# Kernel tuning notes

Hardware: AMD Instinct MI355X
Metric: run time of the kernel (lower is better)

Reference implementation:

```python
import jax, jax.numpy as jnp
import numpy as np

N_CLI, N_AGG, E, D, L = 100000, 1000, 1600000, 128, 3


def setup_inputs() -> dict:
    key = jax.random.key(0)
    ks = jax.random.split(key, 16)
    inp = {
        'x_clients': jax.random.normal(ks[0], (N_CLI, D), jnp.float32),
        'x_agg': jax.random.normal(ks[1], (N_AGG, D), jnp.float32),
        'c2a_src': jax.random.randint(ks[2], (E,), 0, N_CLI, jnp.int32),
        'c2a_dst': jax.random.randint(ks[3], (E,), 0, N_AGG, jnp.int32),
        'a2c_src': jax.random.randint(ks[4], (E,), 0, N_AGG, jnp.int32),
        'a2c_dst': jax.random.randint(ks[5], (E,), 0, N_CLI, jnp.int32),
    }
    s = 1.0 / np.sqrt(D)
    # stacked per-layer SAGE params for each edge type: W_l (on aggregated msg), W_r (on dst), b
    inp['Wl_c2a'] = jax.random.uniform(ks[6], (L, D, D), jnp.float32, -s, s)
    inp['Wr_c2a'] = jax.random.uniform(ks[7], (L, D, D), jnp.float32, -s, s)
    inp['b_c2a'] = jax.random.uniform(ks[8], (L, D), jnp.float32, -s, s)
    inp['Wl_a2c'] = jax.random.uniform(ks[9], (L, D, D), jnp.float32, -s, s)
    inp['Wr_a2c'] = jax.random.uniform(ks[10], (L, D, D), jnp.float32, -s, s)
    inp['b_a2c'] = jax.random.uniform(ks[11], (L, D), jnp.float32, -s, s)
    inp['W_lin'] = jax.random.uniform(ks[12], (D, 1), jnp.float32, -s, s)
    inp['b_lin'] = jax.random.uniform(ks[13], (1,), jnp.float32, -s, s)
    return inp


def _sage(x_src, x_dst, src, dst, Wl, Wr, b, n_dst):
    # mean aggregation of gathered source features onto dst nodes
    msg = x_src[src]                                        # [E, D]
    summed = jax.ops.segment_sum(msg, dst, num_segments=n_dst)
    cnt = jax.ops.segment_sum(jnp.ones((src.shape[0], 1), x_src.dtype), dst, num_segments=n_dst)
    mean = summed / jnp.maximum(cnt, 1.0)
    return mean @ Wl + x_dst @ Wr + b


def _leaky(x):
    return jnp.where(x >= 0, x, 0.1 * x)


def reference(x_clients, x_agg, c2a_src, c2a_dst, a2c_src, a2c_dst,
              Wl_c2a, Wr_c2a, b_c2a, Wl_a2c, Wr_a2c, b_a2c, W_lin, b_lin):
    xc, xa = x_clients, x_agg
    for l in range(L):
        new_a = _sage(xc, xa, c2a_src, c2a_dst, Wl_c2a[l], Wr_c2a[l], b_c2a[l], N_AGG)
        new_c = _sage(xa, xc, a2c_src, a2c_dst, Wl_a2c[l], Wr_a2c[l], b_a2c[l], N_CLI)
        xa, xc = _leaky(new_a), _leaky(new_c)
    return (xc @ W_lin + b_lin).squeeze(1)
```

## Files before the change

### kernel.cpp

```cpp
#include <hip/hip_runtime.h>

#define D      128
#define NCLI   100000
#define NAGG   1000
#define NLAYER 3
#define NBKT   782
#define NRNG   8
#define NBIN   (NAGG * NRNG)
#define RMAGIC 343598u
#define NHIST  512
#define NCVTX  (NCLI * D / 4 / 256)
#define NCVTW  ((NLAYER * D * D + 255) / 256)
#define NROWT  (NCLI / 32)

typedef short bf16x8 __attribute__((ext_vector_type(8)));
typedef float f32x16 __attribute__((ext_vector_type(16)));

static __device__ __forceinline__ float leaky(float x) { return x >= 0.f ? x : 0.1f * x; }

static __device__ __forceinline__ unsigned bf16_rn(float f) {
    unsigned u = __float_as_uint(f);
    return (u + 0x7fffu + ((u >> 16) & 1u)) >> 16;
}
static __device__ __forceinline__ float bf_val(unsigned h) { return __uint_as_float(h << 16); }
static __device__ __forceinline__ unsigned pack_bf2(float lo, float hi) {
    return bf16_rn(lo) | (bf16_rn(hi) << 16);
}
static __device__ __forceinline__ float bf_lo(unsigned v) { return __uint_as_float(v << 16); }
static __device__ __forceinline__ float bf_hi(unsigned v) { return __uint_as_float(v & 0xffff0000u); }

__global__ __launch_bounds__(256) void prep(const int* __restrict__ c2a_src,
                                            const int* __restrict__ c2a_dst,
                                            const int* __restrict__ a2c_dst, int E,
                                            int* __restrict__ cnt_ar, int* __restrict__ bcnt,
                                            const float4* __restrict__ X4,
                                            uint2* __restrict__ xhi, uint2* __restrict__ xlo,
                                            const float* __restrict__ W,
                                            unsigned short* __restrict__ Wt) {
    __shared__ int h[NBIN + NBKT];
    int bid = blockIdx.x;
    if (bid < NHIST) {
        for (int i = threadIdx.x; i < NBIN + NBKT; i += 256) h[i] = 0;
        __syncthreads();
        int stride = NHIST * 256;
        for (int e = bid * 256 + threadIdx.x; e < E; e += stride) {
            int s = c2a_src[e];
            int bin = c2a_dst[e] * NRNG + (int)__umulhi((unsigned)s, RMAGIC);
            atomicAdd(&h[bin], 1);
            atomicAdd(&h[NBIN + (a2c_dst[e] >> 7)], 1);
        }
        __syncthreads();
        for (int i = threadIdx.x; i < NBIN; i += 256)
            if (h[i]) atomicAdd(&cnt_ar[i], h[i]);
        for (int i = threadIdx.x; i < NBKT; i += 256)
            if (h[NBIN + i]) atomicAdd(&bcnt[i], h[NBIN + i]);
    } else if (bid < NHIST + NCVTX) {
        int t = (bid - NHIST) * 256 + threadIdx.x;
        float4 f = X4[t];
        unsigned h0 = bf16_rn(f.x), h1 = bf16_rn(f.y), h2 = bf16_rn(f.z), h3 = bf16_rn(f.w);
        xhi[t] = make_uint2(h0 | (h1 << 16), h2 | (h3 << 16));
        xlo[t] = make_uint2(pack_bf2(f.x - bf_val(h0), f.y - bf_val(h1)),
                            pack_bf2(f.z - bf_val(h2), f.w - bf_val(h3)));
    } else {
        int idx = (bid - NHIST - NCVTX) * 256 + threadIdx.x;
        if (idx >= NLAYER * D * D) return;
        int layer = idx >> 14, rem = idx & (D * D - 1);
        int k = rem >> 7, n = rem & 127;
        float w = W[layer * D * D + k * D + n];
        unsigned hh = bf16_rn(w);
        unsigned short* base = Wt + layer * 2 * D * D;
        base[n * D + k] = (unsigned short)hh;
        base[D * D + n * D + k] = (unsigned short)bf16_rn(w - bf_val(hh));
    }
}

__global__ void scan_both(const int* __restrict__ cnt_ar, int* __restrict__ rp_ar,
                          int* __restrict__ cur_ar, const int* __restrict__ bcnt,
                          int* __restrict__ brp, int* __restrict__ bcur) {
    __shared__ int sh[1024];
    int t = threadIdx.x;
    if (blockIdx.x == 0) {
        int v[8];
        int s = 0;
#pragma unroll
        for (int j = 0; j < 8; j++) {
            int idx = t * 8 + j;
            v[j] = (idx < NBIN) ? cnt_ar[idx] : 0;
            s += v[j];
        }
        sh[t] = s;
        __syncthreads();
        for (int off = 1; off < 1024; off <<= 1) {
            int x = (t >= off) ? sh[t - off] : 0;
            __syncthreads();
            sh[t] += x;
            __syncthreads();
        }
        int run = sh[t] - s;
#pragma unroll
        for (int j = 0; j < 8; j++) {
            int idx = t * 8 + j;
            if (idx < NBIN) {
                rp_ar[idx] = run;
                cur_ar[idx] = run;
            }
            run += v[j];
        }
        if (t == 1023) rp_ar[NBIN] = sh[1023];
    } else {
        int v = (t < NBKT) ? bcnt[t] : 0;
        sh[t] = v;
        __syncthreads();
        for (int off = 1; off < 1024; off <<= 1) {
            int x = (t >= off) ? sh[t - off] : 0;
            __syncthreads();
            sh[t] += x;
            __syncthreads();
        }
        if (t == 0) { brp[0] = 0; bcur[0] = 0; }
        if (t < NBKT) {
            brp[t + 1] = sh[t];
            if (t + 1 < NBKT) bcur[t + 1] = sh[t];
        }
    }
}

__global__ __launch_bounds__(1024) void scatter_both(const int* __restrict__ c2a_src,
                                                     const int* __restrict__ c2a_dst,
                                                     const int* __restrict__ a2c_src,
                                                     const int* __restrict__ a2c_dst, int E,
                                                     int* __restrict__ cur_ar,
                                                     int* __restrict__ col_c2a,
                                                     int* __restrict__ bcur,
                                                     int* __restrict__ sorted1) {
    __shared__ int sbuf[2 * NBIN];
    int tid = threadIdx.x;
    if (blockIdx.x < 256) {
        int* h = sbuf;
        int* base = sbuf + NBIN;
        int chunk = (E + 255) / 256;
        int e0 = blockIdx.x * chunk;
        int e1 = min(E, e0 + chunk);
        for (int i = tid; i < NBIN; i += 1024) h[i] = 0;
        __syncthreads();
        for (int e = e0 + tid; e < e1; e += 1024) {
            int s = c2a_src[e];
            atomicAdd(&h[c2a_dst[e] * NRNG + (int)__umulhi((unsigned)s, RMAGIC)], 1);
        }
        __syncthreads();
        for (int i = tid; i < NBIN; i += 1024) {
            int c = h[i];
            base[i] = c ? atomicAdd(&cur_ar[i], c) : 0;
        }
        __syncthreads();
        for (int e = e0 + tid; e < e1; e += 1024) {
            int s = c2a_src[e];
            int bin = c2a_dst[e] * NRNG + (int)__umulhi((unsigned)s, RMAGIC);
            int pos = atomicAdd(&base[bin], 1);
            col_c2a[pos] = s;
        }
    } else {
        int* h = sbuf;
        int* base = sbuf + NBKT;
        int bid = blockIdx.x - 256;
        int chunk = (E + 255) / 256;
        int e0 = bid * chunk;
        int e1 = min(E, e0 + chunk);
        for (int i = tid; i < NBKT; i += 1024) h[i] = 0;
        __syncthreads();
        for (int e = e0 + tid; e < e1; e += 1024) atomicAdd(&h[a2c_dst[e] >> 7], 1);
        __syncthreads();
        for (int i = tid; i < NBKT; i += 1024) {
            int c = h[i];
            base[i] = c ? atomicAdd(&bcur[i], c) : 0;
        }
        __syncthreads();
        for (int e = e0 + tid; e < e1; e += 1024) {
            int d = a2c_dst[e];
            int pos = atomicAdd(&base[d >> 7], 1);
            sorted1[pos] = ((d & 127) << 10) | a2c_src[e];
        }
    }
}

__global__ __launch_bounds__(512) void bucket_csr(const int* __restrict__ brp,
                                                  const int* __restrict__ sorted1,
                                                  int* __restrict__ rp_c,
                                                  int* __restrict__ col) {
    __shared__ int h[128], cur[128];
    int b = blockIdx.x, tid = threadIdx.x;
    if (tid < 128) h[tid] = 0;
    __syncthreads();
    int beg = brp[b], end = brp[b + 1];
    for (int e = beg + tid; e < end; e += 512) atomicAdd(&h[sorted1[e] >> 10], 1);
    __syncthreads();
    if (tid < 128) cur[tid] = h[tid];
    __syncthreads();
    for (int off = 1; off < 128; off <<= 1) {
        int x = 0;
        if (tid < 128 && tid >= off) x = cur[tid - off];
        __syncthreads();
        if (tid < 128) cur[tid] += x;
        __syncthreads();
    }
    if (tid < 128) {
        int start = beg + cur[tid] - h[tid];
        int c = b * 128 + tid;
        if (c < NCLI) rp_c[c] = start;
        cur[tid] = start;
    }
    if (b == NBKT - 1 && tid == 0) rp_c[NCLI] = end;
    __syncthreads();
    for (int e = beg + tid; e < end; e += 512) {
        int p = sorted1[e];
        int pos = atomicAdd(&cur[p >> 10], 1);
        col[pos] = p & 1023;
    }
}


__global__ __launch_bounds__(512) void gather_mean(const unsigned* __restrict__ tbl,
                                                   const int* __restrict__ rp_ar,
                                                   const int* __restrict__ col,
                                                   float* __restrict__ psum) {
    __shared__ float part[4][8][D];
    int quad = blockIdx.x >> 3, r = blockIdx.x & 7;
    int tid = threadIdx.x;
    int a = tid >> 7;
    int sub = (tid >> 4) & 7;
    int sl = tid & 15;
    const uint4* tbl4 = (const uint4*)tbl;
    int agg = quad * 4 + a;
    int bin = agg * NRNG + r;
    int beg = rp_ar[bin], end = rp_ar[bin + 1];
    float f0 = 0, f1 = 0, f2 = 0, f3 = 0, f4 = 0, f5 = 0, f6 = 0, f7 = 0;
    int e = beg + sub;
    for (; e + 8 < end; e += 16) {
        int s0 = col[e];
        int s1 = col[e + 8];
        uint4 v0 = tbl4[(s0 << 4) + sl];
        uint4 v1 = tbl4[(s1 << 4) + sl];
        f0 += bf_lo(v0.x); f1 += bf_hi(v0.x); f2 += bf_lo(v0.y); f3 += bf_hi(v0.y);
        f4 += bf_lo(v0.z); f5 += bf_hi(v0.z); f6 += bf_lo(v0.w); f7 += bf_hi(v0.w);
        f0 += bf_lo(v1.x); f1 += bf_hi(v1.x); f2 += bf_lo(v1.y); f3 += bf_hi(v1.y);
        f4 += bf_lo(v1.z); f5 += bf_hi(v1.z); f6 += bf_lo(v1.w); f7 += bf_hi(v1.w);
    }
    if (e < end) {
        int s0 = col[e];
        uint4 v0 = tbl4[(s0 << 4) + sl];
        f0 += bf_lo(v0.x); f1 += bf_hi(v0.x); f2 += bf_lo(v0.y); f3 += bf_hi(v0.y);
        f4 += bf_lo(v0.z); f5 += bf_hi(v0.z); f6 += bf_lo(v0.w); f7 += bf_hi(v0.w);
    }
    float* pr = &part[a][sub][sl * 8];
    pr[0] = f0; pr[1] = f1; pr[2] = f2; pr[3] = f3;
    pr[4] = f4; pr[5] = f5; pr[6] = f6; pr[7] = f7;
    __syncthreads();
    int c = tid & 127;
    float s = 0.f;
#pragma unroll
    for (int g = 0; g < 8; g++) s += part[a][g][c];
    psum[((size_t)agg * NRNG + r) * D + c] = s;
}

__global__ __launch_bounds__(128) void combine_agg(const float* __restrict__ psum,
                                                   const int* __restrict__ rp_ar,
                                                   const float* xa_old,
                                                   const float* __restrict__ Wl_a2c,
                                                   const float* __restrict__ Wl_c2a,
                                                   const float* __restrict__ Wr_c2a,
                                                   const float* __restrict__ b_c2a,
                                                   unsigned short* __restrict__ ya_bf,
                                                   float* xa_out) {
    __shared__ float mr[D], xr[D];
    int i = blockIdx.x, j = threadIdx.x;
    const float* pr = psum + (size_t)i * NRNG * D + j;
    float s = 0.f;
#pragma unroll
    for (int r = 0; r < NRNG; r++) s += pr[r * D];
    int deg = rp_ar[i * NRNG + NRNG] - rp_ar[i * NRNG];
    mr[j] = s / fmaxf((float)deg, 1.f);
    xr[j] = xa_old[i * D + j];
    __syncthreads();
    float accy = 0.f, accn = b_c2a[j];
#pragma unroll 4
    for (int k = 0; k < D; k++) {
        accy += xr[k] * Wl_a2c[k * D + j];
        accn += mr[k] * Wl_c2a[k * D + j] + xr[k] * Wr_c2a[k * D + j];
    }
    ya_bf[i * D + j] = (unsigned short)bf16_rn(accy);
    xa_out[i * D + j] = leaky(accn);
}

__global__ __launch_bounds__(256) void gemm_mfma(const unsigned short* __restrict__ Ahi,
                                                 const unsigned short* __restrict__ Alo,
                                                 const unsigned short* __restrict__ Wt,
                                                 const float* __restrict__ bias,
                                                 float* __restrict__ Y) {
    int tid = threadIdx.x;
    int wave = tid >> 6, lane = tid & 63;
    int cl = lane & 31, kh = lane >> 5;
    int n0 = wave * 32;
    const unsigned short* Wlo = Wt + D * D;
    const unsigned short* wbh = Wt + (size_t)(n0 + cl) * D + kh * 8;
    const unsigned short* wbl = Wlo + (size_t)(n0 + cl) * D + kh * 8;
    bf16x8 bhi[8], blo[8];
#pragma unroll
    for (int kc = 0; kc < 8; kc++) {
        bhi[kc] = *(const bf16x8*)(wbh + kc * 16);
        blo[kc] = *(const bf16x8*)(wbl + kc * 16);
    }
    float bv = bias[n0 + cl];
    for (int r = blockIdx.x; r < NROWT; r += gridDim.x) {
        int m0 = r * 32;
        const unsigned short* ar = Ahi + (size_t)(m0 + cl) * D + kh * 8;
        const unsigned short* al = Alo + (size_t)(m0 + cl) * D + kh * 8;
        bf16x8 ahi[8], alo[8];
#pragma unroll
        for (int kc = 0; kc < 8; kc++) {
            ahi[kc] = *(const bf16x8*)(ar + kc * 16);
            alo[kc] = *(const bf16x8*)(al + kc * 16);
        }
        f32x16 acc;
#pragma unroll
        for (int q = 0; q < 16; q++) acc[q] = bv;
#pragma unroll
        for (int kc = 0; kc < 8; kc++) {
            acc = __builtin_amdgcn_mfma_f32_32x32x16_bf16(ahi[kc], bhi[kc], acc, 0, 0, 0);
            acc = __builtin_amdgcn_mfma_f32_32x32x16_bf16(alo[kc], bhi[kc], acc, 0, 0, 0);
            acc = __builtin_amdgcn_mfma_f32_32x32x16_bf16(ahi[kc], blo[kc], acc, 0, 0, 0);
        }
        float* yb = Y + (size_t)m0 * D + n0 + cl;
#pragma unroll
        for (int reg = 0; reg < 16; reg++) {
            int row = (reg & 3) + 8 * (reg >> 2) + 4 * kh;
            yb[(size_t)row * D] = acc[reg];
        }
    }
}

template <int LAST>
__global__ __launch_bounds__(256) void agg_c_bf(const unsigned* __restrict__ ya,
                                                const int* __restrict__ rowptr,
                                                const int* __restrict__ col,
                                                const float* __restrict__ Y,
                                                unsigned* __restrict__ xhi,
                                                unsigned* __restrict__ xlo,
                                                const float* __restrict__ Wlin,
                                                const float* __restrict__ blin,
                                                float* __restrict__ out, int E) {
    int l = threadIdx.x & 63;
    int gid = blockIdx.x * 4 + (threadIdx.x >> 6);
    if (gid >= NCLI) return;
    int beg = rowptr[gid], end = rowptr[gid + 1];
    float a0 = 0, b0 = 0, a1 = 0, b1 = 0, a2 = 0, b2 = 0, a3 = 0, b3 = 0;
    float a4 = 0, b4 = 0, a5 = 0, b5 = 0, a6 = 0, b6 = 0, a7 = 0, b7 = 0;
    for (int ch = beg; ch < end; ch += 64) {
        int len = min(64, end - ch);
        int ec = col[min(ch + l, E - 1)];
        int j = 0;
        for (; j + 8 <= len; j += 8) {
            int r0 = __shfl(ec, j + 0), r1 = __shfl(ec, j + 1);
            int r2 = __shfl(ec, j + 2), r3 = __shfl(ec, j + 3);
            int r4 = __shfl(ec, j + 4), r5 = __shfl(ec, j + 5);
            int r6 = __shfl(ec, j + 6), r7 = __shfl(ec, j + 7);
            unsigned v0 = ya[(r0 << 6) + l];
            unsigned v1 = ya[(r1 << 6) + l];
            unsigned v2 = ya[(r2 << 6) + l];
            unsigned v3 = ya[(r3 << 6) + l];
            unsigned v4 = ya[(r4 << 6) + l];
            unsigned v5 = ya[(r5 << 6) + l];
            unsigned v6 = ya[(r6 << 6) + l];
            unsigned v7 = ya[(r7 << 6) + l];
            a0 += bf_lo(v0); b0 += bf_hi(v0);
            a1 += bf_lo(v1); b1 += bf_hi(v1);
            a2 += bf_lo(v2); b2 += bf_hi(v2);
            a3 += bf_lo(v3); b3 += bf_hi(v3);
            a4 += bf_lo(v4); b4 += bf_hi(v4);
            a5 += bf_lo(v5); b5 += bf_hi(v5);
            a6 += bf_lo(v6); b6 += bf_hi(v6);
            a7 += bf_lo(v7); b7 += bf_hi(v7);
        }
        for (; j < len; j++) {
            int r = __shfl(ec, j);
            unsigned v = ya[(r << 6) + l];
            a0 += bf_lo(v); b0 += bf_hi(v);
        }
    }
    float sx = ((a0 + a1) + (a2 + a3)) + ((a4 + a5) + (a6 + a7));
    float sy = ((b0 + b1) + (b2 + b3)) + ((b4 + b5) + (b6 + b7));
    float inv = 1.f / fmaxf((float)(end - beg), 1.f);
    float2 yv = *(const float2*)&Y[(size_t)gid * D + 2 * l];
    float r0 = leaky(yv.x + sx * inv);
    float r1 = leaky(yv.y + sy * inv);
    if (LAST) {
        float2 w = *(const float2*)&Wlin[2 * l];
        float v = r0 * w.x + r1 * w.y;
#pragma unroll
        for (int off = 32; off > 0; off >>= 1) v += __shfl_down(v, off);
        if (l == 0) out[gid] = v + blin[0];
    } else {
        unsigned h0 = bf16_rn(r0), h1 = bf16_rn(r1);
        xhi[(gid << 6) + l] = h0 | (h1 << 16);
        xlo[(gid << 6) + l] = pack_bf2(r0 - bf_val(h0), r1 - bf_val(h1));
    }
}

extern "C" void kernel_launch(void* const* d_in, const int* in_sizes, int n_in,
                              void* d_out, int out_size, void* d_ws, size_t ws_size,
                              hipStream_t stream) {
    const float* x_clients = (const float*)d_in[0];
    const float* x_agg     = (const float*)d_in[1];
    const int*   c2a_src   = (const int*)d_in[2];
    const int*   c2a_dst   = (const int*)d_in[3];
    const int*   a2c_src   = (const int*)d_in[4];
    const int*   a2c_dst   = (const int*)d_in[5];
    const float* Wl_c2a    = (const float*)d_in[6];
    const float* Wr_c2a    = (const float*)d_in[7];
    const float* b_c2a     = (const float*)d_in[8];
    const float* Wl_a2c    = (const float*)d_in[9];
    const float* Wr_a2c    = (const float*)d_in[10];
    const float* b_a2c     = (const float*)d_in[11];
    const float* W_lin     = (const float*)d_in[12];
    const float* b_lin     = (const float*)d_in[13];
    float* out = (float*)d_out;
    const int E = in_sizes[2];

    char* p = (char*)d_ws;
    auto alloc = [&](size_t bytes) {
        char* r = p;
        p += (bytes + 255) & ~(size_t)255;
        return r;
    };
    float*    Yb    = (float*)alloc(sizeof(float) * NCLI * D);
    unsigned* xc_hi = (unsigned*)alloc(sizeof(unsigned) * NCLI * 64);
    unsigned* xc_lo = (unsigned*)alloc(sizeof(unsigned) * NCLI * 64);
    float*    xa    = (float*)alloc(sizeof(float) * NAGG * D);
    unsigned short* ya_bf = (unsigned short*)alloc(sizeof(unsigned short) * NAGG * D);
    unsigned short* Wt = (unsigned short*)alloc(sizeof(unsigned short) * NLAYER * 2 * D * D);
    float* psum  = (float*)alloc(sizeof(float) * NAGG * NRNG * D);
    int* cnt_ar = (int*)alloc(sizeof(int) * (NBIN + NBKT));
    int* bcnt  = cnt_ar + NBIN;
    int* rp_ar = (int*)alloc(sizeof(int) * (NBIN + 1));
    int* cur_ar = (int*)alloc(sizeof(int) * NBIN);
    int* brp   = (int*)alloc(sizeof(int) * (NBKT + 1));
    int* bcur  = (int*)alloc(sizeof(int) * NBKT);
    int* rp_c  = (int*)alloc(sizeof(int) * (NCLI + 1));
    int* col_c2a = (int*)alloc(sizeof(int) * E);
    int* col_a2c = (int*)alloc(sizeof(int) * E);
    int* sorted1 = (int*)Yb;

    hipMemsetAsync(cnt_ar, 0, sizeof(int) * (NBIN + NBKT), stream);

    prep<<<NHIST + NCVTX + NCVTW, 256, 0, stream>>>(c2a_src, c2a_dst, a2c_dst, E, cnt_ar, bcnt,
                                                    (const float4*)x_clients,
                                                    (uint2*)xc_hi, (uint2*)xc_lo,
                                                    Wr_a2c, Wt);
    scan_both<<<2, 1024, 0, stream>>>(cnt_ar, rp_ar, cur_ar, bcnt, brp, bcur);
    scatter_both<<<512, 1024, 0, stream>>>(c2a_src, c2a_dst, a2c_src, a2c_dst, E,
                                           cur_ar, col_c2a, bcur, sorted1);
    bucket_csr<<<NBKT, 512, 0, stream>>>(brp, sorted1, rp_c, col_a2c);

    const float* xa_old = x_agg;
    for (int l = 0; l < NLAYER; l++) {
        gather_mean<<<(NAGG / 4) * NRNG, 512, 0, stream>>>(xc_hi, rp_ar, col_c2a, psum);
        combine_agg<<<NAGG, 128, 0, stream>>>(psum, rp_ar, xa_old,
                                              Wl_a2c + l * D * D, Wl_c2a + l * D * D,
                                              Wr_c2a + l * D * D, b_c2a + l * D, ya_bf, xa);
        gemm_mfma<<<625, 256, 0, stream>>>(
            (const unsigned short*)xc_hi, (const unsigned short*)xc_lo,
            Wt + l * 2 * D * D, b_a2c + l * D, Yb);
        if (l < NLAYER - 1) {
            agg_c_bf<0><<<(NCLI + 3) / 4, 256, 0, stream>>>((const unsigned*)ya_bf, rp_c, col_a2c,
                                                            Yb, xc_hi, xc_lo, nullptr, nullptr,
                                                            nullptr, E);
        } else {
            agg_c_bf<1><<<(NCLI + 3) / 4, 256, 0, stream>>>((const unsigned*)ya_bf, rp_c, col_a2c,
                                                            Yb, nullptr, nullptr, W_lin, b_lin,
                                                            out, E);
        }
        xa_old = xa;
    }
}
```

Measured before the change: 625.0 us.

## Fuse client GEMM with client-side neighbor aggregation into one kernel

Merges the MFMA GEMM kernel and the client aggregation kernel. The GEMM tile now goes to shared memory instead of a global Y buffer, and each wave then aggregates 8 client rows of the tile in turn. This is meant to remove the write and re-read of the full fp32 Y matrix and one launch per layer. In exchange, the gather work runs on far fewer concurrent waves, since the grid is 625 persistent blocks with sequential per-wave row loops, which may expose more gather latency.

New measurement: 716.3 us. 14.6% more time.

```diff
diff --git a/kernel.cpp b/kernel.cpp
--- a/kernel.cpp
+++ b/kernel.cpp
@@ -291,18 +291,27 @@
     xa_out[i * D + j] = leaky(accn);
 }
 
-__global__ __launch_bounds__(256) void gemm_mfma(const unsigned short* __restrict__ Ahi,
-                                                 const unsigned short* __restrict__ Alo,
-                                                 const unsigned short* __restrict__ Wt,
-                                                 const float* __restrict__ bias,
-                                                 float* __restrict__ Y) {
+template <int LAST>
+__global__ __launch_bounds__(256) void gemm_agg(const unsigned short* __restrict__ Ahi,
+                                                const unsigned short* __restrict__ Alo,
+                                                const unsigned short* __restrict__ Wt,
+                                                const float* __restrict__ bias,
+                                                const unsigned* __restrict__ ya,
+                                                const int* __restrict__ rowptr,
+                                                const int* __restrict__ col,
+                                                unsigned* __restrict__ xhi,
+                                                unsigned* __restrict__ xlo,
+                                                const float* __restrict__ Wlin,
+                                                const float* __restrict__ blin,
+                                                float* __restrict__ out, int E) {
+    __shared__ float smem[32][D];
     int tid = threadIdx.x;
     int wave = tid >> 6, lane = tid & 63;
     int cl = lane & 31, kh = lane >> 5;
     int n0 = wave * 32;
-    const unsigned short* Wlo = Wt + D * D;
+    const unsigned short* Wlo_ = Wt + D * D;
     const unsigned short* wbh = Wt + (size_t)(n0 + cl) * D + kh * 8;
-    const unsigned short* wbl = Wlo + (size_t)(n0 + cl) * D + kh * 8;
+    const unsigned short* wbl = Wlo_ + (size_t)(n0 + cl) * D + kh * 8;
     bf16x8 bhi[8], blo[8];
 #pragma unroll
     for (int kc = 0; kc < 8; kc++) {
@@ -310,6 +319,7 @@
         blo[kc] = *(const bf16x8*)(wbl + kc * 16);
     }
     float bv = bias[n0 + cl];
+    int l = lane;
     for (int r = blockIdx.x; r < NROWT; r += gridDim.x) {
         int m0 = r * 32;
         const unsigned short* ar = Ahi + (size_t)(m0 + cl) * D + kh * 8;
@@ -329,79 +339,69 @@
             acc = __builtin_amdgcn_mfma_f32_32x32x16_bf16(alo[kc], bhi[kc], acc, 0, 0, 0);
             acc = __builtin_amdgcn_mfma_f32_32x32x16_bf16(ahi[kc], blo[kc], acc, 0, 0, 0);
         }
-        float* yb = Y + (size_t)m0 * D + n0 + cl;
 #pragma unroll
         for (int reg = 0; reg < 16; reg++) {
             int row = (reg & 3) + 8 * (reg >> 2) + 4 * kh;
-            yb[(size_t)row * D] = acc[reg];
-        }
-    }
-}
-
-template <int LAST>
-__global__ __launch_bounds__(256) void agg_c_bf(const unsigned* __restrict__ ya,
-                                                const int* __restrict__ rowptr,
-                                                const int* __restrict__ col,
-                                                const float* __restrict__ Y,
-                                                unsigned* __restrict__ xhi,
-                                                unsigned* __restrict__ xlo,
-                                                const float* __restrict__ Wlin,
-                                                const float* __restrict__ blin,
-                                                float* __restrict__ out, int E) {
-    int l = threadIdx.x & 63;
-    int gid = blockIdx.x * 4 + (threadIdx.x >> 6);
-    if (gid >= NCLI) return;
-    int beg = rowptr[gid], end = rowptr[gid + 1];
-    float a0 = 0, b0 = 0, a1 = 0, b1 = 0, a2 = 0, b2 = 0, a3 = 0, b3 = 0;
-    float a4 = 0, b4 = 0, a5 = 0, b5 = 0, a6 = 0, b6 = 0, a7 = 0, b7 = 0;
-    for (int ch = beg; ch < end; ch += 64) {
-        int len = min(64, end - ch);
-        int ec = col[min(ch + l, E - 1)];
-        int j = 0;
-        for (; j + 8 <= len; j += 8) {
-            int r0 = __shfl(ec, j + 0), r1 = __shfl(ec, j + 1);
-            int r2 = __shfl(ec, j + 2), r3 = __shfl(ec, j + 3);
-            int r4 = __shfl(ec, j + 4), r5 = __shfl(ec, j + 5);
-            int r6 = __shfl(ec, j + 6), r7 = __shfl(ec, j + 7);
-            unsigned v0 = ya[(r0 << 6) + l];
-            unsigned v1 = ya[(r1 << 6) + l];
-            unsigned v2 = ya[(r2 << 6) + l];
-            unsigned v3 = ya[(r3 << 6) + l];
-            unsigned v4 = ya[(r4 << 6) + l];
-            unsigned v5 = ya[(r5 << 6) + l];
-            unsigned v6 = ya[(r6 << 6) + l];
-            unsigned v7 = ya[(r7 << 6) + l];
-            a0 += bf_lo(v0); b0 += bf_hi(v0);
-            a1 += bf_lo(v1); b1 += bf_hi(v1);
-            a2 += bf_lo(v2); b2 += bf_hi(v2);
-            a3 += bf_lo(v3); b3 += bf_hi(v3);
-            a4 += bf_lo(v4); b4 += bf_hi(v4);
-            a5 += bf_lo(v5); b5 += bf_hi(v5);
-            a6 += bf_lo(v6); b6 += bf_hi(v6);
-            a7 += bf_lo(v7); b7 += bf_hi(v7);
-        }
-        for (; j < len; j++) {
-            int r = __shfl(ec, j);
-            unsigned v = ya[(r << 6) + l];
-            a0 += bf_lo(v); b0 += bf_hi(v);
-        }
-    }
-    float sx = ((a0 + a1) + (a2 + a3)) + ((a4 + a5) + (a6 + a7));
-    float sy = ((b0 + b1) + (b2 + b3)) + ((b4 + b5) + (b6 + b7));
-    float inv = 1.f / fmaxf((float)(end - beg), 1.f);
-    float2 yv = *(const float2*)&Y[(size_t)gid * D + 2 * l];
-    float r0 = leaky(yv.x + sx * inv);
-    float r1 = leaky(yv.y + sy * inv);
-    if (LAST) {
-        float2 w = *(const float2*)&Wlin[2 * l];
-        float v = r0 * w.x + r1 * w.y;
-#pragma unroll
-        for (int off = 32; off > 0; off >>= 1) v += __shfl_down(v, off);
-        if (l == 0) out[gid] = v + blin[0];
-    } else {
-        unsigned h0 = bf16_rn(r0), h1 = bf16_rn(r1);
-        xhi[(gid << 6) + l] = h0 | (h1 << 16);
-        xlo[(gid << 6) + l] = pack_bf2(r0 - bf_val(h0), r1 - bf_val(h1));
+            smem[row][n0 + cl] = acc[reg];
+        }
+        __syncthreads();
+        for (int i = 0; i < 8; i++) {
+            int c_local = wave * 8 + i;
+            int gid = m0 + c_local;
+            int beg = rowptr[gid], end = rowptr[gid + 1];
+            float a0 = 0, b0 = 0, a1 = 0, b1 = 0, a2 = 0, b2 = 0, a3 = 0, b3 = 0;
+            float a4 = 0, b4 = 0, a5 = 0, b5 = 0, a6 = 0, b6 = 0, a7 = 0, b7 = 0;
+            for (int ch = beg; ch < end; ch += 64) {
+                int len = min(64, end - ch);
+                int ec = col[min(ch + l, E - 1)];
+                int j = 0;
+                for (; j + 8 <= len; j += 8) {
+                    int r0 = __shfl(ec, j + 0), r1 = __shfl(ec, j + 1);
+                    int r2 = __shfl(ec, j + 2), r3 = __shfl(ec, j + 3);
+                    int r4 = __shfl(ec, j + 4), r5 = __shfl(ec, j + 5);
+                    int r6 = __shfl(ec, j + 6), r7 = __shfl(ec, j + 7);
+                    unsigned v0 = ya[(r0 << 6) + l];
+                    unsigned v1 = ya[(r1 << 6) + l];
+                    unsigned v2 = ya[(r2 << 6) + l];
+                    unsigned v3 = ya[(r3 << 6) + l];
+                    unsigned v4 = ya[(r4 << 6) + l];
+                    unsigned v5 = ya[(r5 << 6) + l];
+                    unsigned v6 = ya[(r6 << 6) + l];
+                    unsigned v7 = ya[(r7 << 6) + l];
+                    a0 += bf_lo(v0); b0 += bf_hi(v0);
+                    a1 += bf_lo(v1); b1 += bf_hi(v1);
+                    a2 += bf_lo(v2); b2 += bf_hi(v2);
+                    a3 += bf_lo(v3); b3 += bf_hi(v3);
+                    a4 += bf_lo(v4); b4 += bf_hi(v4);
+                    a5 += bf_lo(v5); b5 += bf_hi(v5);
+                    a6 += bf_lo(v6); b6 += bf_hi(v6);
+                    a7 += bf_lo(v7); b7 += bf_hi(v7);
+                }
+                for (; j < len; j++) {
+                    int rr = __shfl(ec, j);
+                    unsigned v = ya[(rr << 6) + l];
+                    a0 += bf_lo(v); b0 += bf_hi(v);
+                }
+            }
+            float sx = ((a0 + a1) + (a2 + a3)) + ((a4 + a5) + (a6 + a7));
+            float sy = ((b0 + b1) + (b2 + b3)) + ((b4 + b5) + (b6 + b7));
+            float inv = 1.f / fmaxf((float)(end - beg), 1.f);
+            float2 yv = *(const float2*)&smem[c_local][2 * l];
+            float r0 = leaky(yv.x + sx * inv);
+            float r1 = leaky(yv.y + sy * inv);
+            if (LAST) {
+                float2 w = *(const float2*)&Wlin[2 * l];
+                float v = r0 * w.x + r1 * w.y;
+#pragma unroll
+                for (int off = 32; off > 0; off >>= 1) v += __shfl_down(v, off);
+                if (l == 0) out[gid] = v + blin[0];
+            } else {
+                unsigned h0 = bf16_rn(r0), h1 = bf16_rn(r1);
+                xhi[(gid << 6) + l] = h0 | (h1 << 16);
+                xlo[(gid << 6) + l] = pack_bf2(r0 - bf_val(h0), r1 - bf_val(h1));
+            }
+        }
+        __syncthreads();
     }
 }
 
@@ -466,17 +466,16 @@
         combine_agg<<<NAGG, 128, 0, stream>>>(psum, rp_ar, xa_old,
                                               Wl_a2c + l * D * D, Wl_c2a + l * D * D,
                                               Wr_c2a + l * D * D, b_c2a + l * D, ya_bf, xa);
-        gemm_mfma<<<625, 256, 0, stream>>>(
-            (const unsigned short*)xc_hi, (const unsigned short*)xc_lo,
-            Wt + l * 2 * D * D, b_a2c + l * D, Yb);
         if (l < NLAYER - 1) {
-            agg_c_bf<0><<<(NCLI + 3) / 4, 256, 0, stream>>>((const unsigned*)ya_bf, rp_c, col_a2c,
-                                                            Yb, xc_hi, xc_lo, nullptr, nullptr,
-                                                            nullptr, E);
+            gemm_agg<0><<<625, 256, 0, stream>>>(
+                (const unsigned short*)xc_hi, (const unsigned short*)xc_lo,
+                Wt + l * 2 * D * D, b_a2c + l * D, (const unsigned*)ya_bf, rp_c, col_a2c,
+                xc_hi, xc_lo, nullptr, nullptr, nullptr, E);
         } else {
-            agg_c_bf<1><<<(NCLI + 3) / 4, 256, 0, stream>>>((const unsigned*)ya_bf, rp_c, col_a2c,
-                                                            Yb, nullptr, nullptr, W_lin, b_lin,
-                                                            out, E);
+            gemm_agg<1><<<625, 256, 0, stream>>>(
+                (const unsigned short*)xc_hi, (const unsigned short*)xc_lo,
+                Wt + l * 2 * D * D, b_a2c + l * D, (const unsigned*)ya_bf, rp_c, col_a2c,
+                nullptr, nullptr, W_lin, b_lin, out, E);
         }
         xa_old = xa;
     }
```
